# Kernel tuning notes

Measured on AMD Instinct MI355X. Metric: run time of the kernel, lower is better.

The kernel has to match this reference:

```python
import jax, jax.numpy as jnp
import numpy as np

# token_type_vocab constants (closed over; original passes a dict)
WORD_TOKEN, SMILES_TOKEN, VALUE_TOKEN, CLS_TOKEN, SEP_TOKEN, MASK_TOKEN = 0, 1, 2, 3, 4, 5
FP_DIM, HID, COL_VOCAB, MAX_POS, TT_VOCAB = 768, 768, 1000, 512, 8
B, S = 64, 512


def setup_inputs() -> dict:
    key = jax.random.key(0)
    ks = jax.random.split(key, 16)
    scale = 0.02
    return {
        "batch_size": B,
        "max_batch_seq_len": S,
        "SMILES_fps": jax.random.normal(ks[0], (B, S, FP_DIM), jnp.float32),
        "word_tokens_ref": jax.random.randint(ks[1], (B, S), 0, COL_VOCAB),
        "values_ref": jax.random.normal(ks[2], (B, S), jnp.float32),
        "token_type_ids": jax.random.randint(ks[3], (B, S), 0, 6),
        "position_ids": jax.random.randint(ks[4], (B, S), 0, MAX_POS),
        "fc1_w": jax.random.normal(ks[5], (FP_DIM, 4 * FP_DIM), jnp.float32) * scale,
        "fc1_b": jnp.zeros((4 * FP_DIM,), jnp.float32),
        "fc2_w": jax.random.normal(ks[6], (4 * FP_DIM, HID), jnp.float32) * scale,
        "fc2_b": jnp.zeros((HID,), jnp.float32),
        "prop_emb": jax.random.normal(ks[7], (COL_VOCAB, HID), jnp.float32) * scale,
        "val_w": jax.random.normal(ks[8], (HID,), jnp.float32) * scale,  # Linear(1, HID) weight
        "val_b": jnp.zeros((HID,), jnp.float32),
        "pos_emb": jax.random.normal(ks[9], (MAX_POS, HID), jnp.float32) * scale,
        "type_emb": jax.random.normal(ks[10], (TT_VOCAB, HID), jnp.float32) * scale,
        "ln_g": jnp.ones((HID,), jnp.float32),
        "ln_b": jnp.zeros((HID,), jnp.float32),
    }


def reference(batch_size, max_batch_seq_len, SMILES_fps, word_tokens_ref, values_ref,
              token_type_ids, position_ids, fc1_w, fc1_b, fc2_w, fc2_b, prop_emb,
              val_w, val_b, pos_emb, type_emb, ln_g, ln_b):
    word_mask = token_type_ids == WORD_TOKEN
    smiles_mask = token_type_ids == SMILES_TOKEN
    value_mask = token_type_ids == VALUE_TOKEN
    # Faithful to source: '&' of mutually exclusive equalities -> always False
    special_mask = (token_type_ids == CLS_TOKEN) & (token_type_ids == SEP_TOKEN) & (token_type_ids == MASK_TOKEN)

    # branch embeddings computed densely, selected per token (masks are disjoint)
    word_e = prop_emb[word_tokens_ref]                                   # [B,S,H]
    smiles_e = jax.nn.relu(jnp.einsum('bsf,fd->bsd', SMILES_fps, fc1_w) + fc1_b)
    smiles_e = jnp.einsum('bsf,fd->bsd', smiles_e, fc2_w) + fc2_b        # [B,S,H]
    value_e = values_ref[..., None] * val_w + val_b                      # [B,S,H]
    special_e = type_emb[token_type_ids]                                 # [B,S,H]

    input_embeddings = jnp.zeros_like(word_e)
    input_embeddings = jnp.where(word_mask[..., None], word_e, input_embeddings)
    input_embeddings = jnp.where(smiles_mask[..., None], smiles_e, input_embeddings)
    input_embeddings = jnp.where(value_mask[..., None], value_e, input_embeddings)
    input_embeddings = jnp.where(special_mask[..., None], special_e, input_embeddings)

    emb = input_embeddings + pos_emb[position_ids] + type_emb[token_type_ids]
    mu = jnp.mean(emb, axis=-1, keepdims=True)
    var = jnp.mean(jnp.square(emb - mu), axis=-1, keepdims=True)
    emb = (emb - mu) * jax.lax.rsqrt(var + 1e-12) * ln_g + ln_b
    return emb  # dropout_rate=0 (eval): identity
```

## Files before the change

### kernel.cpp

```cpp
#include <hip/hip_runtime.h>
#include <hip/hip_bf16.h>
#include <stdint.h>


typedef __bf16 bf16x8 __attribute__((ext_vector_type(8)));
typedef float f32x4 __attribute__((ext_vector_type(4)));

__device__ __forceinline__ unsigned short f2bf(float f) {
  union { float f; unsigned int u; } c; c.f = f;
  unsigned int u = c.u;
  return (unsigned short)((u + 0x7FFFu + ((u >> 16) & 1u)) >> 16);
}

__global__ void k_compact(const int* __restrict__ tt, int* __restrict__ counter,
                          int* __restrict__ idx, int* __restrict__ slot, int BS) {
  int t = blockIdx.x * 256 + threadIdx.x;
  if (t >= BS) return;
  if (tt[t] == 1) {
    int s = atomicAdd(counter, 1);
    idx[s] = t;
    slot[t] = s;
  }
}

__global__ __launch_bounds__(256) void k_transpose_bf16(
    const float* __restrict__ src, unsigned short* __restrict__ dst, int R, int C) {
  __shared__ float tile[32][33];
  int bx = blockIdx.x * 32;
  int by = blockIdx.y * 32;
  int tx = threadIdx.x & 31;
  int ty = threadIdx.x >> 5;
#pragma unroll
  for (int i = 0; i < 4; i++) {
    int r = by + ty + i * 8;
    tile[ty + i * 8][tx] = src[(size_t)r * C + bx + tx];
  }
  __syncthreads();
#pragma unroll
  for (int i = 0; i < 4; i++) {
    int c = bx + ty + i * 8;
    dst[(size_t)c * R + by + tx] = f2bf(tile[tx][ty + i * 8]);
  }
}

__global__ __launch_bounds__(256) void k_gather(
    const float* __restrict__ fps, const int* __restrict__ idx,
    const int* __restrict__ counter, unsigned short* __restrict__ A1, int cap) {
  int wave = threadIdx.x >> 6, lane = threadIdx.x & 63;
  int s = blockIdx.x * 4 + wave;
  int n = *counter;
  int n_pad = (n + 127) & ~127;
  if (n_pad > cap) n_pad = cap;
  if (s >= n_pad) return;
  ushort4* dst = (ushort4*)(A1 + (size_t)s * 768);
  if (s < n) {
    const float4* srcr = (const float4*)(fps + (size_t)idx[s] * 768);
#pragma unroll
    for (int i = 0; i < 3; i++) {
      float4 v = srcr[lane + (i << 6)];
      ushort4 o;
      o.x = f2bf(v.x); o.y = f2bf(v.y); o.z = f2bf(v.z); o.w = f2bf(v.w);
      dst[lane + (i << 6)] = o;
    }
  } else {
    ushort4 z = {0, 0, 0, 0};
#pragma unroll
    for (int i = 0; i < 3; i++) dst[lane + (i << 6)] = z;
  }
}

template <int MODE, int NB, int KS, int AST, int BST>
__global__ __launch_bounds__(256) void k_gemm(
    const unsigned short* __restrict__ A,
    const unsigned short* __restrict__ BT,
    const float* __restrict__ bias,
    void* __restrict__ C,
    const int* __restrict__ counter, int N, int cap) {
  int n = *counter;
  int n_pad = (n + 127) & ~127;
  if (n_pad > cap) n_pad = cap;
  const int mb = n_pad >> 7;

  constexpr int NCOL = NB * KS;
  constexpr int C_CH = (KS == 4) ? 4 : 2;
  constexpr int A_CH = 8 / C_CH;
  constexpr int CLEN = NCOL / C_CH;

  const int bid = blockIdx.x;
  const int xcd = bid & 7;
  const int j = bid >> 3;
  const int mc = xcd / C_CH, cc = xcd % C_CH;
  const int q = mb / A_CH, r = mb % A_CH;
  const int mlen = q + (mc < r ? 1 : 0);
  const int mbase = mc * q + (mc < r ? mc : r);
  if (j >= mlen * CLEN) return;
  const int m_blk = mbase + j / CLEN;
  const int c_blk = cc * CLEN + j % CLEN;
  const int ks = c_blk / NB;
  const int nb = c_blk % NB;
  const int m0 = m_blk * 128, n0 = nb * 128;
  const int k0g = ks * 768;

  __shared__ __attribute__((aligned(128))) char smem[65536];
  auto lds = (__attribute__((address_space(3))) char*)smem;

  const int t = threadIdx.x;
  const int wave = t >> 6;
  const int lane = t & 63;
  const int wm = (wave >> 1) * 64;
  const int wn = (wave & 1) * 64;

  f32x4 acc[4][4] = {};

  auto stage = [&](int kk0, int bufbase) {
#pragma unroll
    for (int i = 0; i < 4; i++) {
      int c = i * 256 + t;
      int rr = c >> 3;
      int k8 = (c & 7) ^ (rr & 7);
      const unsigned short* ga = A + (size_t)(m0 + rr) * AST + kk0 + k8 * 8;
      __builtin_amdgcn_global_load_lds(
          (const __attribute__((address_space(1))) void*)ga,
          (__attribute__((address_space(3))) void*)(lds + bufbase + i * 4096 + wave * 1024),
          16, 0, 0);
    }
#pragma unroll
    for (int i = 0; i < 4; i++) {
      int c = i * 256 + t;
      int rr = c >> 3;
      int k8 = (c & 7) ^ (rr & 7);
      const unsigned short* gb = BT + (size_t)(n0 + rr) * BST + kk0 + k8 * 8;
      __builtin_amdgcn_global_load_lds(
          (const __attribute__((address_space(1))) void*)gb,
          (__attribute__((address_space(3))) void*)(lds + bufbase + 16384 + i * 4096 + wave * 1024),
          16, 0, 0);
    }
  };

  stage(k0g, 0);
  __syncthreads();
  int cur = 0;

  for (int it = 0; it < 12; ++it) {
    if (it + 1 < 12) stage(k0g + (it + 1) * 64, (cur ^ 1) * 32768);
    const int bufbase = cur * 32768;
#pragma unroll
    for (int kk = 0; kk < 2; kk++) {
      bf16x8 af[4], bfr[4];
      int kbyte = (kk * 32 + ((lane >> 4) * 8)) * 2;
#pragma unroll
      for (int mi = 0; mi < 4; mi++) {
        int rr = wm + mi * 16 + (lane & 15);
        af[mi] = *(const bf16x8*)(smem + bufbase + rr * 128 + (kbyte ^ ((rr & 7) << 4)));
      }
#pragma unroll
      for (int ni = 0; ni < 4; ni++) {
        int rr = wn + ni * 16 + (lane & 15);
        bfr[ni] = *(const bf16x8*)(smem + bufbase + 16384 + rr * 128 + (kbyte ^ ((rr & 7) << 4)));
      }
#pragma unroll
      for (int mi = 0; mi < 4; mi++)
#pragma unroll
        for (int ni = 0; ni < 4; ni++)
          acc[mi][ni] = __builtin_amdgcn_mfma_f32_16x16x32_bf16(
              af[mi], bfr[ni], acc[mi][ni], 0, 0, 0);
    }
    __syncthreads();
    cur ^= 1;
  }

#pragma unroll
  for (int ni = 0; ni < 4; ni++) {
    int col = n0 + wn + ni * 16 + (lane & 15);
    float bv = (MODE == 1) ? bias[col] : 0.f;
#pragma unroll
    for (int mi = 0; mi < 4; mi++) {
#pragma unroll
      for (int j2 = 0; j2 < 4; j2++) {
        int row = m0 + wm + mi * 16 + ((lane >> 4) * 4) + j2;
        float v = acc[mi][ni][j2] + bv;
        if constexpr (MODE == 1) {
          v = v > 0.f ? v : 0.f;
          ((unsigned short*)C)[(size_t)row * N + col] = f2bf(v);
        } else {
          ((float*)C)[((size_t)ks * cap + row) * N + col] = v;
        }
      }
    }
  }
}

template <int KS>
__global__ __launch_bounds__(256) void k_assemble(
    const float* __restrict__ sout, const float* __restrict__ fc2b,
    const int* __restrict__ slot,
    const int* __restrict__ ttid, const int* __restrict__ word,
    const float* __restrict__ values, const int* __restrict__ posid,
    const float* __restrict__ prop, const float* __restrict__ valw,
    const float* __restrict__ valb, const float* __restrict__ pose,
    const float* __restrict__ tye, const float* __restrict__ lng,
    const float* __restrict__ lnb, float* __restrict__ out, int BS, int cap) {
  int wave = threadIdx.x >> 6, lane = threadIdx.x & 63;
  int t = blockIdx.x * 4 + wave;
  if (t >= BS) return;
  int tt = ttid[t];

  float v[12];
  if (tt == 1) {
    int sl = slot[t];
    const float4* pr[KS];
#pragma unroll
    for (int p = 0; p < KS; p++)
      pr[p] = (const float4*)(sout + ((size_t)p * cap + sl) * 768);
    const float4* b4 = (const float4*)fc2b;
#pragma unroll
    for (int i = 0; i < 3; i++) {
      float4 x = pr[0][lane + (i << 6)];
#pragma unroll
      for (int p = 1; p < KS; p++) {
        float4 y = pr[p][lane + (i << 6)];
        x.x += y.x; x.y += y.y; x.z += y.z; x.w += y.w;
      }
      float4 b = b4[lane + (i << 6)];
      v[4 * i] = x.x + b.x; v[4 * i + 1] = x.y + b.y;
      v[4 * i + 2] = x.z + b.z; v[4 * i + 3] = x.w + b.w;
    }
  } else if (tt == 0) {
    const float4* row = (const float4*)(prop + (size_t)word[t] * 768);
#pragma unroll
    for (int i = 0; i < 3; i++) {
      float4 x = row[lane + (i << 6)];
      v[4 * i] = x.x; v[4 * i + 1] = x.y; v[4 * i + 2] = x.z; v[4 * i + 3] = x.w;
    }
  } else if (tt == 2) {
    float val = values[t];
#pragma unroll
    for (int i = 0; i < 3; i++) {
      float4 w = ((const float4*)valw)[lane + (i << 6)];
      float4 b = ((const float4*)valb)[lane + (i << 6)];
      v[4 * i] = val * w.x + b.x; v[4 * i + 1] = val * w.y + b.y;
      v[4 * i + 2] = val * w.z + b.z; v[4 * i + 3] = val * w.w + b.w;
    }
  } else {
#pragma unroll
    for (int j = 0; j < 12; j++) v[j] = 0.f;
  }

  const float4* p4 = (const float4*)(pose + (size_t)posid[t] * 768);
  const float4* ty4 = (const float4*)(tye + (size_t)tt * 768);
#pragma unroll
  for (int i = 0; i < 3; i++) {
    float4 p = p4[lane + (i << 6)];
    float4 y = ty4[lane + (i << 6)];
    v[4 * i] += p.x + y.x; v[4 * i + 1] += p.y + y.y;
    v[4 * i + 2] += p.z + y.z; v[4 * i + 3] += p.w + y.w;
  }

  float s = 0.f;
#pragma unroll
  for (int j = 0; j < 12; j++) s += v[j];
#pragma unroll
  for (int o = 32; o >= 1; o >>= 1) s += __shfl_xor(s, o);
  float mu = s * (1.0f / 768.0f);

  float qv = 0.f;
#pragma unroll
  for (int j = 0; j < 12; j++) { float d = v[j] - mu; qv += d * d; }
#pragma unroll
  for (int o = 32; o >= 1; o >>= 1) qv += __shfl_xor(qv, o);
  float rs = 1.0f / sqrtf(qv * (1.0f / 768.0f) + 1e-12f);

  float4* o4 = (float4*)(out + (size_t)t * 768);
#pragma unroll
  for (int i = 0; i < 3; i++) {
    float4 g = ((const float4*)lng)[lane + (i << 6)];
    float4 b = ((const float4*)lnb)[lane + (i << 6)];
    float4 r;
    r.x = (v[4 * i] - mu) * rs * g.x + b.x;
    r.y = (v[4 * i + 1] - mu) * rs * g.y + b.y;
    r.z = (v[4 * i + 2] - mu) * rs * g.z + b.z;
    r.w = (v[4 * i + 3] - mu) * rs * g.w + b.w;
    o4[lane + (i << 6)] = r;
  }
}

extern "C" void kernel_launch(void* const* d_in, const int* in_sizes, int n_in,
                              void* d_out, int out_size, void* d_ws, size_t ws_size,
                              hipStream_t stream) {
  const int BS = in_sizes[3];
  const float* fps    = (const float*)d_in[2];
  const int*   word   = (const int*)d_in[3];
  const float* values = (const float*)d_in[4];
  const int*   tt     = (const int*)d_in[5];
  const int*   pos    = (const int*)d_in[6];
  const float* fc1_w  = (const float*)d_in[7];
  const float* fc1_b  = (const float*)d_in[8];
  const float* fc2_w  = (const float*)d_in[9];
  const float* fc2_b  = (const float*)d_in[10];
  const float* prop   = (const float*)d_in[11];
  const float* valw   = (const float*)d_in[12];
  const float* valb   = (const float*)d_in[13];
  const float* pose   = (const float*)d_in[14];
  const float* tye    = (const float*)d_in[15];
  const float* lng    = (const float*)d_in[16];
  const float* lnb    = (const float*)d_in[17];
  float* out = (float*)d_out;

  char* ws = (char*)d_ws;
  const size_t off_idx  = 256;
  const size_t off_slot = off_idx + (size_t)BS * 4;
  const size_t off_w1t  = off_slot + (size_t)BS * 4;
  const size_t off_w2t  = off_w1t + (size_t)768 * 3072 * 2;
  const size_t off_A1   = off_w2t + (size_t)3072 * 768 * 2;
  const size_t fixed    = off_A1;
  size_t avail = ws_size > fixed ? ws_size - fixed : 0;

  const size_t per_tok4 = 768 * 2 + 3072 * 2 + 4 * 768 * 4;
  const bool splitk = avail >= (size_t)8192 * per_tok4;

  int cap, KSn;
  if (splitk) {
    cap = 8192; KSn = 4;
  } else {
    const size_t per_tok1 = 768 * 2 + 3072 * 2 + 768 * 4;
    long c = (long)(avail / per_tok1);
    c &= ~511L;
    if (c > BS) c = BS;
    if (c < 512) c = 512;
    cap = (int)c; KSn = 1;
  }
  const int MBcap = cap / 128;

  const size_t off_h1   = off_A1 + (size_t)cap * 768 * 2;
  const size_t off_sout = off_h1 + (size_t)cap * 3072 * 2;

  int* counter = (int*)(ws + 0);
  int* idx     = (int*)(ws + off_idx);
  int* slot    = (int*)(ws + off_slot);
  unsigned short* w1t = (unsigned short*)(ws + off_w1t);
  unsigned short* w2t = (unsigned short*)(ws + off_w2t);
  unsigned short* A1  = (unsigned short*)(ws + off_A1);
  unsigned short* h1  = (unsigned short*)(ws + off_h1);
  float* sout = (float*)(ws + off_sout);

  hipMemsetAsync(counter, 0, 4, stream);
  k_compact<<<(BS + 255) / 256, 256, 0, stream>>>(tt, counter, idx, slot, BS);
  k_transpose_bf16<<<dim3(3072 / 32, 768 / 32), 256, 0, stream>>>(fc1_w, w1t, 768, 3072);
  k_transpose_bf16<<<dim3(768 / 32, 3072 / 32), 256, 0, stream>>>(fc2_w, w2t, 3072, 768);
  k_gather<<<cap / 4, 256, 0, stream>>>(fps, idx, counter, A1, cap);

  k_gemm<1, 24, 1, 768, 768><<<24 * MBcap, 256, 0, stream>>>(
      A1, w1t, fc1_b, (void*)h1, counter, 3072, cap);

  if (splitk) {
    k_gemm<0, 6, 4, 3072, 3072><<<24 * MBcap, 256, 0, stream>>>(
        h1, w2t, nullptr, (void*)sout, counter, 768, cap);
    k_assemble<4><<<(BS + 3) / 4, 256, 0, stream>>>(
        sout, fc2_b, slot, tt, word, values, pos, prop, valw, valb, pose, tye,
        lng, lnb, out, BS, cap);
  } else {
    k_gemm<0, 6, 1, 3072, 3072><<<6 * MBcap, 256, 0, stream>>>(
        h1, w2t, nullptr, (void*)sout, counter, 768, cap);
    k_assemble<1><<<(BS + 3) / 4, 256, 0, stream>>>(
        sout, fc2_b, slot, tt, word, values, pos, prop, valw, valb, pose, tye,
        lng, lnb, out, BS, cap);
  }
}
```

Measured before the change: 138.9 us.

## Store split-K partials in bf16 and fuse weight transposes with counter reset

The split-K partial outputs of the second GEMM are now written as bf16 instead of fp32, and the assemble kernel upconverts and sums them. This halves the partial-sum write and read traffic. Separately, the two weight-transpose launches and the counter memset are merged into one prep kernel to cut launch overhead. The cost is lower precision in the partial sums before layernorm.

Measured after the change: 124.6 us. 1.12x faster.

```diff
diff --git a/kernel.cpp b/kernel.cpp
--- a/kernel.cpp
+++ b/kernel.cpp
@@ -10,6 +10,43 @@
   union { float f; unsigned int u; } c; c.f = f;
   unsigned int u = c.u;
   return (unsigned short)((u + 0x7FFFu + ((u >> 16) & 1u)) >> 16);
+}
+__device__ __forceinline__ float bf2f(unsigned short b) {
+  union { unsigned int u; float f; } c; c.u = ((unsigned int)b) << 16;
+  return c.f;
+}
+
+__global__ __launch_bounds__(256) void k_prep(
+    const float* __restrict__ fc1_w, const float* __restrict__ fc2_w,
+    unsigned short* __restrict__ w1t, unsigned short* __restrict__ w2t,
+    int* __restrict__ counter) {
+  if (blockIdx.x == 0 && threadIdx.x == 0) *counter = 0;
+  __shared__ float tile[32][33];
+  int b = blockIdx.x;
+  const float* src;
+  unsigned short* dst;
+  int R, C, bx, by;
+  if (b < 2304) {
+    src = fc1_w; dst = w1t; R = 768; C = 3072;
+    bx = (b % 96) * 32; by = (b / 96) * 32;
+  } else {
+    b -= 2304;
+    src = fc2_w; dst = w2t; R = 3072; C = 768;
+    bx = (b % 24) * 32; by = (b / 24) * 32;
+  }
+  int tx = threadIdx.x & 31;
+  int ty = threadIdx.x >> 5;
+#pragma unroll
+  for (int i = 0; i < 4; i++) {
+    int r = by + ty + i * 8;
+    tile[ty + i * 8][tx] = src[(size_t)r * C + bx + tx];
+  }
+  __syncthreads();
+#pragma unroll
+  for (int i = 0; i < 4; i++) {
+    int c = bx + ty + i * 8;
+    dst[(size_t)c * R + by + tx] = f2bf(tile[tx][ty + i * 8]);
+  }
 }
 
 __global__ void k_compact(const int* __restrict__ tt, int* __restrict__ counter,
@@ -20,26 +57,6 @@
     int s = atomicAdd(counter, 1);
     idx[s] = t;
     slot[t] = s;
-  }
-}
-
-__global__ __launch_bounds__(256) void k_transpose_bf16(
-    const float* __restrict__ src, unsigned short* __restrict__ dst, int R, int C) {
-  __shared__ float tile[32][33];
-  int bx = blockIdx.x * 32;
-  int by = blockIdx.y * 32;
-  int tx = threadIdx.x & 31;
-  int ty = threadIdx.x >> 5;
-#pragma unroll
-  for (int i = 0; i < 4; i++) {
-    int r = by + ty + i * 8;
-    tile[ty + i * 8][tx] = src[(size_t)r * C + bx + tx];
-  }
-  __syncthreads();
-#pragma unroll
-  for (int i = 0; i < 4; i++) {
-    int c = bx + ty + i * 8;
-    dst[(size_t)c * R + by + tx] = f2bf(tile[tx][ty + i * 8]);
   }
 }
 
@@ -74,7 +91,7 @@
     const unsigned short* __restrict__ A,
     const unsigned short* __restrict__ BT,
     const float* __restrict__ bias,
-    void* __restrict__ C,
+    unsigned short* __restrict__ C,
     const int* __restrict__ counter, int N, int cap) {
   int n = *counter;
   int n_pad = (n + 127) & ~127;
@@ -181,9 +198,9 @@
         float v = acc[mi][ni][j2] + bv;
         if constexpr (MODE == 1) {
           v = v > 0.f ? v : 0.f;
-          ((unsigned short*)C)[(size_t)row * N + col] = f2bf(v);
+          C[(size_t)row * N + col] = f2bf(v);
         } else {
-          ((float*)C)[((size_t)ks * cap + row) * N + col] = v;
+          C[((size_t)ks * cap + row) * N + col] = f2bf(v);
         }
       }
     }
@@ -192,7 +209,7 @@
 
 template <int KS>
 __global__ __launch_bounds__(256) void k_assemble(
-    const float* __restrict__ sout, const float* __restrict__ fc2b,
+    const unsigned short* __restrict__ sout, const float* __restrict__ fc2b,
     const int* __restrict__ slot,
     const int* __restrict__ ttid, const int* __restrict__ word,
     const float* __restrict__ values, const int* __restrict__ posid,
@@ -208,22 +225,21 @@
   float v[12];
   if (tt == 1) {
     int sl = slot[t];
-    const float4* pr[KS];
+    const ushort4* pr[KS];
 #pragma unroll
     for (int p = 0; p < KS; p++)
-      pr[p] = (const float4*)(sout + ((size_t)p * cap + sl) * 768);
+      pr[p] = (const ushort4*)(sout + ((size_t)p * cap + sl) * 768);
     const float4* b4 = (const float4*)fc2b;
 #pragma unroll
     for (int i = 0; i < 3; i++) {
-      float4 x = pr[0][lane + (i << 6)];
-#pragma unroll
-      for (int p = 1; p < KS; p++) {
-        float4 y = pr[p][lane + (i << 6)];
-        x.x += y.x; x.y += y.y; x.z += y.z; x.w += y.w;
+      float4 b = b4[lane + (i << 6)];
+      float a0 = b.x, a1 = b.y, a2 = b.z, a3 = b.w;
+#pragma unroll
+      for (int p = 0; p < KS; p++) {
+        ushort4 u = pr[p][lane + (i << 6)];
+        a0 += bf2f(u.x); a1 += bf2f(u.y); a2 += bf2f(u.z); a3 += bf2f(u.w);
       }
-      float4 b = b4[lane + (i << 6)];
-      v[4 * i] = x.x + b.x; v[4 * i + 1] = x.y + b.y;
-      v[4 * i + 2] = x.z + b.z; v[4 * i + 3] = x.w + b.w;
+      v[4 * i] = a0; v[4 * i + 1] = a1; v[4 * i + 2] = a2; v[4 * i + 3] = a3;
     }
   } else if (tt == 0) {
     const float4* row = (const float4*)(prop + (size_t)word[t] * 768);
@@ -315,19 +331,19 @@
   const size_t fixed    = off_A1;
   size_t avail = ws_size > fixed ? ws_size - fixed : 0;
 
-  const size_t per_tok4 = 768 * 2 + 3072 * 2 + 4 * 768 * 4;
+  const size_t per_tok4 = 768 * 2 + 3072 * 2 + 4 * 768 * 2;
   const bool splitk = avail >= (size_t)8192 * per_tok4;
 
-  int cap, KSn;
+  int cap;
   if (splitk) {
-    cap = 8192; KSn = 4;
-  } else {
-    const size_t per_tok1 = 768 * 2 + 3072 * 2 + 768 * 4;
+    cap = 8192;
+  } else {
+    const size_t per_tok1 = 768 * 2 + 3072 * 2 + 768 * 2;
     long c = (long)(avail / per_tok1);
     c &= ~511L;
     if (c > BS) c = BS;
     if (c < 512) c = 512;
-    cap = (int)c; KSn = 1;
+    cap = (int)c;
   }
   const int MBcap = cap / 128;
 
@@ -341,26 +357,24 @@
   unsigned short* w2t = (unsigned short*)(ws + off_w2t);
   unsigned short* A1  = (unsigned short*)(ws + off_A1);
   unsigned short* h1  = (unsigned short*)(ws + off_h1);
-  float* sout = (float*)(ws + off_sout);
-
-  hipMemsetAsync(counter, 0, 4, stream);
+  unsigned short* sout = (unsigned short*)(ws + off_sout);
+
+  k_prep<<<4608, 256, 0, stream>>>(fc1_w, fc2_w, w1t, w2t, counter);
   k_compact<<<(BS + 255) / 256, 256, 0, stream>>>(tt, counter, idx, slot, BS);
-  k_transpose_bf16<<<dim3(3072 / 32, 768 / 32), 256, 0, stream>>>(fc1_w, w1t, 768, 3072);
-  k_transpose_bf16<<<dim3(768 / 32, 3072 / 32), 256, 0, stream>>>(fc2_w, w2t, 3072, 768);
   k_gather<<<cap / 4, 256, 0, stream>>>(fps, idx, counter, A1, cap);
 
   k_gemm<1, 24, 1, 768, 768><<<24 * MBcap, 256, 0, stream>>>(
-      A1, w1t, fc1_b, (void*)h1, counter, 3072, cap);
+      A1, w1t, fc1_b, h1, counter, 3072, cap);
 
   if (splitk) {
     k_gemm<0, 6, 4, 3072, 3072><<<24 * MBcap, 256, 0, stream>>>(
-        h1, w2t, nullptr, (void*)sout, counter, 768, cap);
+        h1, w2t, nullptr, sout, counter, 768, cap);
     k_assemble<4><<<(BS + 3) / 4, 256, 0, stream>>>(
         sout, fc2_b, slot, tt, word, values, pos, prop, valw, valb, pose, tye,
         lng, lnb, out, BS, cap);
   } else {
     k_gemm<0, 6, 1, 3072, 3072><<<6 * MBcap, 256, 0, stream>>>(
-        h1, w2t, nullptr, (void*)sout, counter, 768, cap);
+        h1, w2t, nullptr, sout, counter, 768, cap);
     k_assemble<1><<<(BS + 3) / 4, 256, 0, stream>>>(
         sout, fc2_b, slot, tt, word, values, pos, prop, valw, valb, pose, tye,
         lng, lnb, out, BS, cap);
```
